# Optimization experiments

Hardware: AMD Instinct MI355X
Metric: run time of the kernel (lower is better)

Reference implementation:

```python
import jax, jax.numpy as jnp
import numpy as np
import math

CH = 256
NH = 8
HD = CH // NH
GROUPS = 32
EPS = 1e-5


def group_norm(x, gamma, beta):
    # x: [B, C, H, W]; normalize over (C//GROUPS, H, W) per group
    B, C, H, W = x.shape
    xg = x.reshape(B, GROUPS, C // GROUPS, H, W)
    mean = xg.mean(axis=(2, 3, 4), keepdims=True)
    var = xg.var(axis=(2, 3, 4), keepdims=True)
    xg = (xg - mean) * jax.lax.rsqrt(var + EPS)
    x = xg.reshape(B, C, H, W)
    return x * gamma[None, :, None, None] + beta[None, :, None, None]


def setup_inputs() -> dict:
    key = jax.random.key(0)
    ks = jax.random.split(key, 7)
    B, H, W = 2, 64, 64
    x = jax.random.normal(ks[0], (B, CH, H, W), dtype=jnp.float32)
    # conv1x1 weights stored as [out, in] (kernel 1x1 squeezed)
    w_qkv = jax.random.normal(ks[1], (3 * CH, CH), dtype=jnp.float32) * (1.0 / math.sqrt(CH))
    b_qkv = jax.random.normal(ks[2], (3 * CH,), dtype=jnp.float32) * 0.01
    w_proj = jax.random.normal(ks[3], (CH, CH), dtype=jnp.float32) * (1.0 / math.sqrt(CH))
    b_proj = jax.random.normal(ks[4], (CH,), dtype=jnp.float32) * 0.01
    gn_gamma = jnp.ones((CH,), dtype=jnp.float32)
    gn_beta = jnp.zeros((CH,), dtype=jnp.float32)
    return {"x": x, "w_qkv": w_qkv, "b_qkv": b_qkv, "w_proj": w_proj,
            "b_proj": b_proj, "gn_gamma": gn_gamma, "gn_beta": gn_beta}


def reference(x, w_qkv, b_qkv, w_proj, b_proj, gn_gamma, gn_beta):
    B, C, H, W = x.shape
    HW = H * W
    h = group_norm(x, gn_gamma, gn_beta)
    # 1x1 conv == channel matmul
    qkv = jnp.einsum('bchw,oc->bohw', h, w_qkv) + b_qkv[None, :, None, None]
    q, k, v = jnp.split(qkv, 3, axis=1)  # each [B, C, H, W]
    # reshape to heads: q,v -> [B, NH, HW, HD]; k -> [B, NH, HD, HW]
    q = q.reshape(B, NH, HD, HW).transpose(0, 1, 3, 2)
    k = k.reshape(B, NH, HD, HW)
    v = v.reshape(B, NH, HD, HW).transpose(0, 1, 3, 2)
    scale = 1.0 / math.sqrt(HD)
    attn = jnp.einsum('bnqd,bndk->bnqk', q, k) * scale  # [B, NH, HW, HW]
    attn = jax.nn.softmax(attn, axis=-1)
    out = jnp.einsum('bnqk,bnkd->bnqd', attn, v)  # [B, NH, HW, HD]
    out = out.transpose(0, 1, 3, 2).reshape(B, C, H, W)
    out = jnp.einsum('bchw,oc->bohw', out, w_proj) + b_proj[None, :, None, None]
    return x + out
```

## Files before the change

### kernel.cpp

```cpp
#include <hip/hip_runtime.h>
#include <hip/hip_bf16.h>


typedef __attribute__((ext_vector_type(8))) __bf16 bf16x8;
typedef __attribute__((ext_vector_type(4))) float f32x4;
typedef __attribute__((ext_vector_type(2))) float f32x2;
typedef __attribute__((ext_vector_type(16))) float f32x16;
typedef __attribute__((ext_vector_type(2))) unsigned int uint32x2;

#define HW 4096
#define C 256
#define NH 8
#define HD 32
#define QSCALE 0.25505654f
#define KST 36
#define VST 68
#define TST 36
#define NSPLIT 4

__device__ inline unsigned short f2bf(float f) {
  union { float f; unsigned int u; } v; v.f = f;
  unsigned int u = v.u;
  return (unsigned short)((u + 0x7fffu + ((u >> 16) & 1u)) >> 16);
}

__device__ inline bf16x8 load8(const unsigned short* p) {
  bf16x8 v;
  __builtin_memcpy(&v, __builtin_assume_aligned(p, 16), 16);
  return v;
}

__device__ inline bf16x8 load8_lds(const unsigned short* p) {
  uint2 a = *(const uint2*)__builtin_assume_aligned(p, 8);
  uint2 b = *(const uint2*)__builtin_assume_aligned(p + 4, 8);
  union { uint4 u; bf16x8 v; } cv;
  cv.u = make_uint4(a.x, a.y, b.x, b.y);
  return cv.v;
}

__device__ inline unsigned int fbits(float f) {
  unsigned int u; __builtin_memcpy(&u, &f, 4); return u;
}
__device__ inline float bits2f(unsigned int u) {
  float f; __builtin_memcpy(&f, &u, 4); return f;
}

__device__ inline unsigned int pack_bf2(float lo, float hi) {
  return __builtin_amdgcn_perm(fbits(hi) + 0x8000u, fbits(lo) + 0x8000u, 0x07060302u);
}
__device__ inline unsigned int pack_bf2t(float lo, float hi) {
  return __builtin_amdgcn_perm(fbits(hi), fbits(lo), 0x07060302u);
}

__device__ inline size_t toff(int row, int col) {
  return ((size_t)(row >> 6) * 8 + (col >> 5)) * 2048 + (row & 63) * 32 + (col & 31);
}

__global__ __launch_bounds__(256) void gn_stats_part(const float* __restrict__ x,
                                                     float* __restrict__ parts,
                                                     const float* __restrict__ wq,
                                                     const float* __restrict__ wp,
                                                     unsigned short* __restrict__ wq_t,
                                                     unsigned short* __restrict__ wp_t) {
  if (blockIdx.x >= 256) {
    int base = (blockIdx.x - 256) * 1024 + threadIdx.x * 4;
    #pragma unroll
    for (int k = 0; k < 4; k++) {
      int idx = base + k;
      if (idx < 196608) {
        int o = idx >> 8, c = idx & 255;
        wq_t[toff(o, c)] = f2bf(wq[idx]);
      } else {
        int i2 = idx - 196608;
        int o = i2 >> 8, c = i2 & 255;
        wp_t[toff(o, c)] = f2bf(wp[i2]);
      }
    }
    return;
  }
  int i = blockIdx.x;
  const float4* p4 = (const float4*)(x + (size_t)i * 8192);
  int t = threadIdx.x;
  float s = 0.f, ss = 0.f;
  for (int k = t; k < 2048; k += 256) {
    float4 v = p4[k];
    s  += v.x + v.y + v.z + v.w;
    ss += v.x*v.x + v.y*v.y + v.z*v.z + v.w*v.w;
  }
  for (int m = 32; m >= 1; m >>= 1) {
    s  += __shfl_down(s, m, 64);
    ss += __shfl_down(ss, m, 64);
  }
  __shared__ float red[8];
  int w = t >> 6;
  if ((t & 63) == 0) { red[w] = s; red[w + 4] = ss; }
  __syncthreads();
  if (t == 0) {
    parts[i]       = red[0] + red[1] + red[2] + red[3];
    parts[256 + i] = red[4] + red[5] + red[6] + red[7];
  }
}

__global__ __launch_bounds__(256) void gn_apply(const float* __restrict__ x,
                                                const float* __restrict__ parts,
                                                const float* __restrict__ gamma,
                                                const float* __restrict__ beta,
                                                unsigned short* __restrict__ h_t) {
  __shared__ float tile[64][65];
  __shared__ float gmean[8], grstd[8];
  int b = blockIdx.z, c0 = blockIdx.y * 64, s0 = blockIdx.x * 64;
  int t = threadIdx.x;
  if (t < 8) {
    int bg = b * 32 + (c0 >> 3) + t;
    float s  = (parts[4*bg] + parts[4*bg+1]) + (parts[4*bg+2] + parts[4*bg+3]);
    float ss = (parts[256+4*bg] + parts[256+4*bg+1]) + (parts[256+4*bg+2] + parts[256+4*bg+3]);
    float mean = s * (1.0f / 32768.0f);
    float var  = ss * (1.0f / 32768.0f) - mean * mean;
    gmean[t] = mean;
    grstd[t] = rsqrtf(var + 1e-5f);
  }
  const float* xb = x + ((size_t)b * C + c0) * HW + s0;
  #pragma unroll
  for (int k = 0; k < 16; k++) {
    int e = k * 256 + t;
    int i = e >> 6, j = e & 63;
    tile[i][j] = xb[(size_t)i * HW + j];
  }
  __syncthreads();
  unsigned short* hb = h_t + (size_t)b * HW * C +
                       ((size_t)(s0 >> 6) * 8 + (c0 >> 5)) * 2048;
  #pragma unroll
  for (int k = 0; k < 16; k++) {
    int e = k * 256 + t;
    int jr = e >> 6, ir = e & 63;
    int c = c0 + ir, gl = ir >> 3;
    float v = (tile[ir][jr] - gmean[gl]) * grstd[gl] * gamma[c] + beta[c];
    hb[(ir >> 5) * 2048 + jr * 32 + (ir & 31)] = f2bf(v);
  }
}

__global__ __launch_bounds__(256) void qkv_gemm(const unsigned short* __restrict__ wq_t,
                                                const unsigned short* __restrict__ h_t,
                                                const float* __restrict__ b_qkv,
                                                unsigned short* __restrict__ q_t,
                                                unsigned short* __restrict__ k_t,
                                                unsigned short* __restrict__ v_t) {
  int t = threadIdx.x;
  int lane = t & 63, w = t >> 6;
  int quad = lane >> 4, l16 = lane & 15;
  int m0 = blockIdx.y * 64 + w * 16;
  int n0 = blockIdx.x * 64;
  int b  = blockIdx.z;

  __shared__ __align__(16) unsigned short at2[2][64 * TST];
  __shared__ __align__(16) unsigned short bt2[2][64 * TST];

  const uint4* Ag = (const uint4*)(wq_t + (size_t)blockIdx.y * 8 * 2048);
  const uint4* Bg = (const uint4*)(h_t + (size_t)b * HW * C + (size_t)blockIdx.x * 8 * 2048);
  int lrow = t >> 2, lcol = (t & 3) * 8;

  f32x4 acc[4];
  #pragma unroll
  for (int nb = 0; nb < 4; nb++) acc[nb] = (f32x4){0.f, 0.f, 0.f, 0.f};

  uint4 areg = Ag[t];
  uint4 breg = Bg[t];
  int phase = 0;
  for (int k = 0; k < 8; k++, phase ^= 1) {
    unsigned short* ap = &at2[phase][0];
    unsigned short* bp = &bt2[phase][0];
    *(uint2*)(ap + lrow * TST + lcol)     = make_uint2(areg.x, areg.y);
    *(uint2*)(ap + lrow * TST + lcol + 4) = make_uint2(areg.z, areg.w);
    *(uint2*)(bp + lrow * TST + lcol)     = make_uint2(breg.x, breg.y);
    *(uint2*)(bp + lrow * TST + lcol + 4) = make_uint2(breg.z, breg.w);
    int kn = (k < 7) ? k + 1 : 7;
    areg = Ag[kn * 256 + t];
    breg = Bg[kn * 256 + t];
    __syncthreads();
    bf16x8 a = load8_lds(ap + (w * 16 + l16) * TST + quad * 8);
    #pragma unroll
    for (int nb = 0; nb < 4; nb++) {
      bf16x8 bb = load8_lds(bp + (nb * 16 + l16) * TST + quad * 8);
      acc[nb] = __builtin_amdgcn_mfma_f32_16x16x32_bf16(a, bb, acc[nb], 0, 0, 0);
    }
  }

  int seg = m0 >> 8;
  int o0 = m0 + quad * 4;
  #pragma unroll
  for (int nb = 0; nb < 4; nb++) {
    int s = n0 + nb * 16 + l16;
    if (seg == 2) {
      #pragma unroll
      for (int r = 0; r < 4; r++)
        v_t[((size_t)b * C + ((o0 + r) - 512)) * HW + s] = f2bf(acc[nb][r] + b_qkv[o0 + r]);
    } else {
      float sc = seg ? 1.0f : QSCALE;
      float v0 = (acc[nb][0] + b_qkv[o0])     * sc;
      float v1 = (acc[nb][1] + b_qkv[o0 + 1]) * sc;
      float v2 = (acc[nb][2] + b_qkv[o0 + 2]) * sc;
      float v3 = (acc[nb][3] + b_qkv[o0 + 3]) * sc;
      int oc = o0 & 255, h = oc >> 5, d = oc & 31;
      unsigned short* dst = seg ? k_t : q_t;
      uint2 dd;
      dd.x = pack_bf2(v0, v1);
      dd.y = pack_bf2(v2, v3);
      *(uint2*)(dst + (((size_t)b * NH + h) * HW + s) * HD + d) = dd;
    }
  }
}

__device__ __forceinline__ void softmax_frag(const f32x16& S, f32x2& ps2,
                                             bf16x8& f0, bf16x8& f1) {
  float p[16];
  #pragma unroll
  for (int r = 0; r < 16; r++)
    p[r] = __builtin_amdgcn_exp2f(S[r]);
  f32x2 t0 = (f32x2){p[0], p[1]} + (f32x2){p[2], p[3]};
  f32x2 t1 = (f32x2){p[4], p[5]} + (f32x2){p[6], p[7]};
  f32x2 t2 = (f32x2){p[8], p[9]} + (f32x2){p[10], p[11]};
  f32x2 t3 = (f32x2){p[12], p[13]} + (f32x2){p[14], p[15]};
  ps2 += (t0 + t1) + (t2 + t3);
  unsigned int c0 = pack_bf2t(p[0],  p[1]);
  unsigned int c1 = pack_bf2t(p[2],  p[3]);
  unsigned int c2 = pack_bf2t(p[4],  p[5]);
  unsigned int c3 = pack_bf2t(p[6],  p[7]);
  unsigned int c4 = pack_bf2t(p[8],  p[9]);
  unsigned int c5 = pack_bf2t(p[10], p[11]);
  unsigned int c6 = pack_bf2t(p[12], p[13]);
  unsigned int c7 = pack_bf2t(p[14], p[15]);
  uint32x2 s02 = __builtin_amdgcn_permlane32_swap(c0, c2, false, false);
  uint32x2 s13 = __builtin_amdgcn_permlane32_swap(c1, c3, false, false);
  uint32x2 s46 = __builtin_amdgcn_permlane32_swap(c4, c6, false, false);
  uint32x2 s57 = __builtin_amdgcn_permlane32_swap(c5, c7, false, false);
  union { uint4 u; bf16x8 v; } a, b;
  a.u = make_uint4(s02.x, s13.x, s02.y, s13.y);
  b.u = make_uint4(s46.x, s57.x, s46.y, s57.y);
  f0 = a.v;
  f1 = b.v;
}

__global__ __launch_bounds__(256) void flash_part(const unsigned short* __restrict__ q_t,
                                                  const unsigned short* __restrict__ k_t,
                                                  const unsigned short* __restrict__ v_t,
                                                  unsigned short* __restrict__ po,
                                                  float* __restrict__ pl,
                                                  int jspan) {
  int t = threadIdx.x;
  int lane = t & 63, w = t >> 6;
  int n = lane & 31, hi = lane >> 5, hi8 = hi * 8;
  int bh = blockIdx.x, b = bh >> 3, h = bh & 7;
  int m0 = blockIdx.y * 128 + w * 32;
  int z = blockIdx.z;

  __shared__ __align__(16) unsigned short kt2[2][64 * KST];
  __shared__ __align__(16) unsigned short vt2[2][32 * VST];

  const unsigned short* Q  = q_t + (size_t)bh * HW * HD;
  const unsigned short* Kg = k_t + (size_t)bh * HW * HD;
  const unsigned short* Vg = v_t + ((size_t)b * C + h * HD) * HW;

  bf16x8 qf0 = load8(Q + (size_t)(m0 + n) * HD + hi8);
  bf16x8 qf1 = load8(Q + (size_t)(m0 + n) * HD + 16 + hi8);

  int kkey = t >> 2, kseg = (t & 3) * 8;
  int vd   = t >> 3, vseg = (t & 7) * 8;
  const unsigned short* kgp = Kg + (size_t)kkey * HD + kseg;
  const unsigned short* vgp = Vg + (size_t)vd * HW + vseg;

  f32x2 ps2 = (f32x2){0.f, 0.f};
  f32x16 oT = (f32x16){0.f,0.f,0.f,0.f,0.f,0.f,0.f,0.f,0.f,0.f,0.f,0.f,0.f,0.f,0.f,0.f};
  const f32x16 zero16 = (f32x16){0.f,0.f,0.f,0.f,0.f,0.f,0.f,0.f,0.f,0.f,0.f,0.f,0.f,0.f,0.f,0.f};

  int jbase = z * jspan, jend = jbase + jspan;
  uint4 kreg = *(const uint4*)(kgp + (size_t)jbase * HD);
  uint4 vreg = *(const uint4*)(vgp + jbase);

  int phase = 0;
  for (int j0 = jbase; j0 < jend; j0 += 64, phase ^= 1) {
    unsigned short* ktp = &kt2[phase][0];
    unsigned short* vtp = &vt2[phase][0];
    *(uint2*)(ktp + kkey * KST + kseg)     = make_uint2(kreg.x, kreg.y);
    *(uint2*)(ktp + kkey * KST + kseg + 4) = make_uint2(kreg.z, kreg.w);
    *(uint2*)(vtp + vd * VST + vseg)       = make_uint2(vreg.x, vreg.y);
    *(uint2*)(vtp + vd * VST + vseg + 4)   = make_uint2(vreg.z, vreg.w);
    int jn = (j0 + 64 < jend) ? (j0 + 64) : jbase;
    kreg = *(const uint4*)(kgp + (size_t)jn * HD);
    vreg = *(const uint4*)(vgp + jn);
    __syncthreads();

    const unsigned short* kr0 = ktp + n * KST;
    const unsigned short* kr1 = ktp + (32 + n) * KST;
    bf16x8 ka0 = load8_lds(kr0 + hi8);
    bf16x8 ka1 = load8_lds(kr0 + 16 + hi8);
    bf16x8 kb0 = load8_lds(kr1 + hi8);
    bf16x8 kb1 = load8_lds(kr1 + 16 + hi8);
    f32x16 S0 = __builtin_amdgcn_mfma_f32_32x32x16_bf16(ka1, qf1, zero16, 0, 0, 0);
    S0 = __builtin_amdgcn_mfma_f32_32x32x16_bf16(ka0, qf0, S0, 0, 0, 0);
    f32x16 S1 = __builtin_amdgcn_mfma_f32_32x32x16_bf16(kb1, qf1, zero16, 0, 0, 0);
    S1 = __builtin_amdgcn_mfma_f32_32x32x16_bf16(kb0, qf0, S1, 0, 0, 0);
    bf16x8 pf0, pf1, pf2, pf3;
    softmax_frag(S0, ps2, pf0, pf1);
    softmax_frag(S1, ps2, pf2, pf3);
    const unsigned short* vrow = vtp + n * VST;
    bf16x8 vf0 = load8_lds(vrow + hi8);
    bf16x8 vf1 = load8_lds(vrow + 16 + hi8);
    bf16x8 vf2 = load8_lds(vrow + 32 + hi8);
    bf16x8 vf3 = load8_lds(vrow + 48 + hi8);
    oT = __builtin_amdgcn_mfma_f32_32x32x16_bf16(vf0, pf0, oT, 0, 0, 0);
    oT = __builtin_amdgcn_mfma_f32_32x32x16_bf16(vf1, pf1, oT, 0, 0, 0);
    oT = __builtin_amdgcn_mfma_f32_32x32x16_bf16(vf2, pf2, oT, 0, 0, 0);
    oT = __builtin_amdgcn_mfma_f32_32x32x16_bf16(vf3, pf3, oT, 0, 0, 0);
  }

  float psum = ps2.x + ps2.y;
  psum += __shfl_xor(psum, 32, 64);

  unsigned short* pr = po + (((size_t)z * 16 + bh) * HW + (m0 + n)) * 32;
  #pragma unroll
  for (int g = 0; g < 4; g++) {
    uint2 dd;
    dd.x = pack_bf2(oT[4 * g], oT[4 * g + 1]);
    dd.y = pack_bf2(oT[4 * g + 2], oT[4 * g + 3]);
    *(uint2*)(pr + g * 8 + hi * 4) = dd;
  }
  if (lane < 32)
    pl[((size_t)z * 16 + bh) * HW + m0 + n] = psum;
}

__global__ __launch_bounds__(256) void merge_parts(const unsigned short* __restrict__ po,
                                                   const float* __restrict__ pl,
                                                   unsigned short* __restrict__ ao_t) {
  int g = blockIdx.x * 256 + threadIdx.x;
  int q4 = g & 3, s = (g >> 2) & 4095, bh = g >> 14;
  const uint4* p4 = (const uint4*)po;
  size_t idx = ((size_t)bh * HW + s) * 4 + q4;
  const size_t zstride = (size_t)16 * HW * 4;
  float acc[8] = {0,0,0,0,0,0,0,0};
  float l = 0.f;
  #pragma unroll
  for (int z = 0; z < NSPLIT; z++) {
    uint4 v = p4[z * zstride + idx];
    acc[0] += bits2f(v.x << 16);  acc[1] += bits2f(v.x & 0xffff0000u);
    acc[2] += bits2f(v.y << 16);  acc[3] += bits2f(v.y & 0xffff0000u);
    acc[4] += bits2f(v.z << 16);  acc[5] += bits2f(v.z & 0xffff0000u);
    acc[6] += bits2f(v.w << 16);  acc[7] += bits2f(v.w & 0xffff0000u);
    l += pl[((size_t)z * 16 + bh) * HW + s];
  }
  float inv = 1.0f / l;
  int b = bh >> 3, h = bh & 7;
  uint4 o;
  o.x = pack_bf2(acc[0] * inv, acc[1] * inv);
  o.y = pack_bf2(acc[2] * inv, acc[3] * inv);
  o.z = pack_bf2(acc[4] * inv, acc[5] * inv);
  o.w = pack_bf2(acc[6] * inv, acc[7] * inv);
  *(uint4*)(ao_t + (size_t)b * HW * C +
            ((size_t)(s >> 6) * 8 + h) * 2048 + (s & 63) * 32 + q4 * 8) = o;
}

__global__ __launch_bounds__(256) void proj_gemm(const unsigned short* __restrict__ wp_t,
                                                 const unsigned short* __restrict__ ao_t,
                                                 const float* __restrict__ b_proj,
                                                 const float* __restrict__ x,
                                                 float* __restrict__ out) {
  int t = threadIdx.x;
  int lane = t & 63, w = t >> 6;
  int quad = lane >> 4, l16 = lane & 15;
  int m0 = blockIdx.y * 64 + w * 16;
  int n0 = blockIdx.x * 64;
  int b  = blockIdx.z;

  __shared__ __align__(16) unsigned short at2[2][64 * TST];
  __shared__ __align__(16) unsigned short bt2[2][64 * TST];

  const uint4* Ag = (const uint4*)(wp_t + (size_t)blockIdx.y * 8 * 2048);
  const uint4* Bg = (const uint4*)(ao_t + (size_t)b * HW * C + (size_t)blockIdx.x * 8 * 2048);
  int lrow = t >> 2, lcol = (t & 3) * 8;

  f32x4 acc[4];
  #pragma unroll
  for (int nb = 0; nb < 4; nb++) acc[nb] = (f32x4){0.f, 0.f, 0.f, 0.f};

  uint4 areg = Ag[t];
  uint4 breg = Bg[t];
  int phase = 0;
  for (int k = 0; k < 8; k++, phase ^= 1) {
    unsigned short* ap = &at2[phase][0];
    unsigned short* bp = &bt2[phase][0];
    *(uint2*)(ap + lrow * TST + lcol)     = make_uint2(areg.x, areg.y);
    *(uint2*)(ap + lrow * TST + lcol + 4) = make_uint2(areg.z, areg.w);
    *(uint2*)(bp + lrow * TST + lcol)     = make_uint2(breg.x, breg.y);
    *(uint2*)(bp + lrow * TST + lcol + 4) = make_uint2(breg.z, breg.w);
    int kn = (k < 7) ? k + 1 : 7;
    areg = Ag[kn * 256 + t];
    breg = Bg[kn * 256 + t];
    __syncthreads();
    bf16x8 a = load8_lds(ap + (w * 16 + l16) * TST + quad * 8);
    #pragma unroll
    for (int nb = 0; nb < 4; nb++) {
      bf16x8 bb = load8_lds(bp + (nb * 16 + l16) * TST + quad * 8);
      acc[nb] = __builtin_amdgcn_mfma_f32_16x16x32_bf16(a, bb, acc[nb], 0, 0, 0);
    }
  }
  #pragma unroll
  for (int nb = 0; nb < 4; nb++) {
    int s = n0 + nb * 16 + l16;
    #pragma unroll
    for (int r = 0; r < 4; r++) {
      int o = m0 + quad * 4 + r;
      size_t idx = ((size_t)b * C + o) * HW + s;
      out[idx] = acc[nb][r] + b_proj[o] + x[idx];
    }
  }
}

extern "C" void kernel_launch(void* const* d_in, const int* in_sizes, int n_in,
                              void* d_out, int out_size, void* d_ws, size_t ws_size,
                              hipStream_t stream) {
  const float* x      = (const float*)d_in[0];
  const float* w_qkv  = (const float*)d_in[1];
  const float* b_qkv  = (const float*)d_in[2];
  const float* w_proj = (const float*)d_in[3];
  const float* b_proj = (const float*)d_in[4];
  const float* gamma  = (const float*)d_in[5];
  const float* beta   = (const float*)d_in[6];
  float* out = (float*)d_out;

  char* ws = (char*)d_ws;
  float*          parts = (float*)ws;
  unsigned short* wq_t  = (unsigned short*)(ws + 4096);
  unsigned short* wp_t  = (unsigned short*)(ws + 397312);
  unsigned short* h_t   = (unsigned short*)(ws + 528384);
  unsigned short* q_t   = (unsigned short*)(ws + 4722688);
  unsigned short* k_t   = (unsigned short*)(ws + 8916992);
  unsigned short* v_t   = (unsigned short*)(ws + 13111296);
  unsigned short* po    = (unsigned short*)(ws + 17305600);
  float*          pl    = (float*)(ws + 34082816);
  unsigned short* ao_t  = h_t;

  gn_stats_part<<<512, 256, 0, stream>>>(x, parts, w_qkv, w_proj, wq_t, wp_t);
  gn_apply<<<dim3(64, 4, 2), 256, 0, stream>>>(x, parts, gamma, beta, h_t);
  qkv_gemm<<<dim3(64, 12, 2), 256, 0, stream>>>(wq_t, h_t, b_qkv, q_t, k_t, v_t);
  flash_part<<<dim3(16, 32, NSPLIT), 256, 0, stream>>>(q_t, k_t, v_t, po, pl, HW / NSPLIT);
  merge_parts<<<1024, 256, 0, stream>>>(po, pl, ao_t);
  proj_gemm<<<dim3(64, 4, 2), 256, 0, stream>>>(wp_t, ao_t, b_proj, x, out);
}
```

Baseline: 156.4 us.

## Process two 32-query tiles per warp in flash attention to reuse K/V fragments

Each warp now handles 64 query rows (two 32-row tiles) instead of 32, reusing the K and V fragments loaded from LDS for both tiles. The grid's query dimension is halved, so there are half as many blocks and half the K/V global-to-LDS staging traffic per query. The cost is more registers per thread (two output accumulators and extra Q fragments), possibly lower occupancy, and 1024 blocks instead of 2048, which reduces parallelism.

New measurement: 151.7 us. 1.03x faster.

```diff
diff --git a/kernel.cpp b/kernel.cpp
--- a/kernel.cpp
+++ b/kernel.cpp
@@ -250,7 +250,7 @@
   int lane = t & 63, w = t >> 6;
   int n = lane & 31, hi = lane >> 5, hi8 = hi * 8;
   int bh = blockIdx.x, b = bh >> 3, h = bh & 7;
-  int m0 = blockIdx.y * 128 + w * 32;
+  int m0 = blockIdx.y * 256 + w * 64;
   int z = blockIdx.z;
 
   __shared__ __align__(16) unsigned short kt2[2][64 * KST];
@@ -260,16 +260,20 @@
   const unsigned short* Kg = k_t + (size_t)bh * HW * HD;
   const unsigned short* Vg = v_t + ((size_t)b * C + h * HD) * HW;
 
-  bf16x8 qf0 = load8(Q + (size_t)(m0 + n) * HD + hi8);
-  bf16x8 qf1 = load8(Q + (size_t)(m0 + n) * HD + 16 + hi8);
+  bf16x8 qa0 = load8(Q + (size_t)(m0 + n) * HD + hi8);
+  bf16x8 qa1 = load8(Q + (size_t)(m0 + n) * HD + 16 + hi8);
+  bf16x8 qb0 = load8(Q + (size_t)(m0 + 32 + n) * HD + hi8);
+  bf16x8 qb1 = load8(Q + (size_t)(m0 + 32 + n) * HD + 16 + hi8);
 
   int kkey = t >> 2, kseg = (t & 3) * 8;
   int vd   = t >> 3, vseg = (t & 7) * 8;
   const unsigned short* kgp = Kg + (size_t)kkey * HD + kseg;
   const unsigned short* vgp = Vg + (size_t)vd * HW + vseg;
 
-  f32x2 ps2 = (f32x2){0.f, 0.f};
-  f32x16 oT = (f32x16){0.f,0.f,0.f,0.f,0.f,0.f,0.f,0.f,0.f,0.f,0.f,0.f,0.f,0.f,0.f,0.f};
+  f32x2 psa = (f32x2){0.f, 0.f};
+  f32x2 psb = (f32x2){0.f, 0.f};
+  f32x16 oTa = (f32x16){0.f,0.f,0.f,0.f,0.f,0.f,0.f,0.f,0.f,0.f,0.f,0.f,0.f,0.f,0.f,0.f};
+  f32x16 oTb = (f32x16){0.f,0.f,0.f,0.f,0.f,0.f,0.f,0.f,0.f,0.f,0.f,0.f,0.f,0.f,0.f,0.f};
   const f32x16 zero16 = (f32x16){0.f,0.f,0.f,0.f,0.f,0.f,0.f,0.f,0.f,0.f,0.f,0.f,0.f,0.f,0.f,0.f};
 
   int jbase = z * jspan, jend = jbase + jspan;
@@ -295,37 +299,58 @@
     bf16x8 ka1 = load8_lds(kr0 + 16 + hi8);
     bf16x8 kb0 = load8_lds(kr1 + hi8);
     bf16x8 kb1 = load8_lds(kr1 + 16 + hi8);
-    f32x16 S0 = __builtin_amdgcn_mfma_f32_32x32x16_bf16(ka1, qf1, zero16, 0, 0, 0);
-    S0 = __builtin_amdgcn_mfma_f32_32x32x16_bf16(ka0, qf0, S0, 0, 0, 0);
-    f32x16 S1 = __builtin_amdgcn_mfma_f32_32x32x16_bf16(kb1, qf1, zero16, 0, 0, 0);
-    S1 = __builtin_amdgcn_mfma_f32_32x32x16_bf16(kb0, qf0, S1, 0, 0, 0);
+
+    f32x16 S0 = __builtin_amdgcn_mfma_f32_32x32x16_bf16(ka1, qa1, zero16, 0, 0, 0);
+    S0 = __builtin_amdgcn_mfma_f32_32x32x16_bf16(ka0, qa0, S0, 0, 0, 0);
+    f32x16 S1 = __builtin_amdgcn_mfma_f32_32x32x16_bf16(kb1, qa1, zero16, 0, 0, 0);
+    S1 = __builtin_amdgcn_mfma_f32_32x32x16_bf16(kb0, qa0, S1, 0, 0, 0);
     bf16x8 pf0, pf1, pf2, pf3;
-    softmax_frag(S0, ps2, pf0, pf1);
-    softmax_frag(S1, ps2, pf2, pf3);
+    softmax_frag(S0, psa, pf0, pf1);
+    softmax_frag(S1, psa, pf2, pf3);
     const unsigned short* vrow = vtp + n * VST;
     bf16x8 vf0 = load8_lds(vrow + hi8);
     bf16x8 vf1 = load8_lds(vrow + 16 + hi8);
     bf16x8 vf2 = load8_lds(vrow + 32 + hi8);
     bf16x8 vf3 = load8_lds(vrow + 48 + hi8);
-    oT = __builtin_amdgcn_mfma_f32_32x32x16_bf16(vf0, pf0, oT, 0, 0, 0);
-    oT = __builtin_amdgcn_mfma_f32_32x32x16_bf16(vf1, pf1, oT, 0, 0, 0);
-    oT = __builtin_amdgcn_mfma_f32_32x32x16_bf16(vf2, pf2, oT, 0, 0, 0);
-    oT = __builtin_amdgcn_mfma_f32_32x32x16_bf16(vf3, pf3, oT, 0, 0, 0);
-  }
-
-  float psum = ps2.x + ps2.y;
-  psum += __shfl_xor(psum, 32, 64);
-
-  unsigned short* pr = po + (((size_t)z * 16 + bh) * HW + (m0 + n)) * 32;
+    oTa = __builtin_amdgcn_mfma_f32_32x32x16_bf16(vf0, pf0, oTa, 0, 0, 0);
+    oTa = __builtin_amdgcn_mfma_f32_32x32x16_bf16(vf1, pf1, oTa, 0, 0, 0);
+    oTa = __builtin_amdgcn_mfma_f32_32x32x16_bf16(vf2, pf2, oTa, 0, 0, 0);
+    oTa = __builtin_amdgcn_mfma_f32_32x32x16_bf16(vf3, pf3, oTa, 0, 0, 0);
+
+    f32x16 T0 = __builtin_amdgcn_mfma_f32_32x32x16_bf16(ka1, qb1, zero16, 0, 0, 0);
+    T0 = __builtin_amdgcn_mfma_f32_32x32x16_bf16(ka0, qb0, T0, 0, 0, 0);
+    f32x16 T1 = __builtin_amdgcn_mfma_f32_32x32x16_bf16(kb1, qb1, zero16, 0, 0, 0);
+    T1 = __builtin_amdgcn_mfma_f32_32x32x16_bf16(kb0, qb0, T1, 0, 0, 0);
+    softmax_frag(T0, psb, pf0, pf1);
+    softmax_frag(T1, psb, pf2, pf3);
+    oTb = __builtin_amdgcn_mfma_f32_32x32x16_bf16(vf0, pf0, oTb, 0, 0, 0);
+    oTb = __builtin_amdgcn_mfma_f32_32x32x16_bf16(vf1, pf1, oTb, 0, 0, 0);
+    oTb = __builtin_amdgcn_mfma_f32_32x32x16_bf16(vf2, pf2, oTb, 0, 0, 0);
+    oTb = __builtin_amdgcn_mfma_f32_32x32x16_bf16(vf3, pf3, oTb, 0, 0, 0);
+  }
+
+  float psuma = psa.x + psa.y;
+  psuma += __shfl_xor(psuma, 32, 64);
+  float psumb = psb.x + psb.y;
+  psumb += __shfl_xor(psumb, 32, 64);
+
+  unsigned short* pra = po + (((size_t)z * 16 + bh) * HW + (m0 + n)) * 32;
+  unsigned short* prb = po + (((size_t)z * 16 + bh) * HW + (m0 + 32 + n)) * 32;
   #pragma unroll
   for (int g = 0; g < 4; g++) {
     uint2 dd;
-    dd.x = pack_bf2(oT[4 * g], oT[4 * g + 1]);
-    dd.y = pack_bf2(oT[4 * g + 2], oT[4 * g + 3]);
-    *(uint2*)(pr + g * 8 + hi * 4) = dd;
-  }
-  if (lane < 32)
-    pl[((size_t)z * 16 + bh) * HW + m0 + n] = psum;
+    dd.x = pack_bf2(oTa[4 * g], oTa[4 * g + 1]);
+    dd.y = pack_bf2(oTa[4 * g + 2], oTa[4 * g + 3]);
+    *(uint2*)(pra + g * 8 + hi * 4) = dd;
+    uint2 de;
+    de.x = pack_bf2(oTb[4 * g], oTb[4 * g + 1]);
+    de.y = pack_bf2(oTb[4 * g + 2], oTb[4 * g + 3]);
+    *(uint2*)(prb + g * 8 + hi * 4) = de;
+  }
+  if (lane < 32) {
+    pl[((size_t)z * 16 + bh) * HW + m0 + n] = psuma;
+    pl[((size_t)z * 16 + bh) * HW + m0 + 32 + n] = psumb;
+  }
 }
 
 __global__ __launch_bounds__(256) void merge_parts(const unsigned short* __restrict__ po,
@@ -441,7 +466,7 @@
   gn_stats_part<<<512, 256, 0, stream>>>(x, parts, w_qkv, w_proj, wq_t, wp_t);
   gn_apply<<<dim3(64, 4, 2), 256, 0, stream>>>(x, parts, gamma, beta, h_t);
   qkv_gemm<<<dim3(64, 12, 2), 256, 0, stream>>>(wq_t, h_t, b_qkv, q_t, k_t, v_t);
-  flash_part<<<dim3(16, 32, NSPLIT), 256, 0, stream>>>(q_t, k_t, v_t, po, pl, HW / NSPLIT);
+  flash_part<<<dim3(16, 16, NSPLIT), 256, 0, stream>>>(q_t, k_t, v_t, po, pl, HW / NSPLIT);
   merge_parts<<<1024, 256, 0, stream>>>(po, pl, ao_t);
   proj_gemm<<<dim3(64, 4, 2), 256, 0, stream>>>(wp_t, ao_t, b_proj, x, out);
 }
```
